# Kernel tuning notes

Hardware: AMD Instinct MI355X
Metric: run time of the kernel (lower is better)

Reference implementation:

```python
import jax, jax.numpy as jnp
import numpy as np

SEG = 4      # segment_size
H = 8        # n_heads
D = 1024     # d_model
B = 8
S = 4096


def setup_inputs() -> dict:
    key = jax.random.key(0)
    ks = jax.random.split(key, 9)
    s = 0.02  # init scale for weights
    return {
        "x": jax.random.normal(ks[0], (B, S, D), dtype=jnp.float32),
        "proj_qk_w": jax.random.normal(ks[1], (D, D), dtype=jnp.float32) * s,
        "proj_qk_b": jax.random.normal(ks[2], (D,), dtype=jnp.float32) * s,
        "proj_v_w": jax.random.normal(ks[3], (D, D), dtype=jnp.float32) * s,
        "proj_v_b": jax.random.normal(ks[4], (D,), dtype=jnp.float32) * s,
        "in_proj_w": jax.random.normal(ks[5], (3 * D, D), dtype=jnp.float32) * s,
        "in_proj_b": jax.random.normal(ks[6], (3 * D,), dtype=jnp.float32) * s,
        "out_proj_w": jax.random.normal(ks[7], (D, D), dtype=jnp.float32) * s,
        "out_proj_b": jax.random.normal(ks[8], (D,), dtype=jnp.float32) * s,
    }


def reference(x, proj_qk_w, proj_qk_b, proj_v_w, proj_v_b,
              in_proj_w, in_proj_b, out_proj_w, out_proj_b):
    b, seq_len, d = x.shape
    hd = d // H
    # torch: pad = seg - S % seg  (pads a full segment when S % seg == 0)
    pad = SEG - seq_len % SEG
    x = jnp.concatenate([x, x[:, :pad]], axis=1)          # [b, T, d]
    T = seq_len + pad
    a = T // SEG
    # cat(chunk(x, a, dim=1), dim=0): block-major stacking -> [a*b, SEG, d]
    xb = x.reshape(b, a, SEG, d).transpose(1, 0, 2, 3).reshape(a * b, SEG, d)

    # extra projections (same qk projection used for query and key)
    qk_in = xb @ proj_qk_w.T + proj_qk_b                   # [a*b, SEG, d]
    v_in = xb @ proj_v_w.T + proj_v_b

    # nn.MultiheadAttention in-projection
    wq, wk, wv = jnp.split(in_proj_w, 3, axis=0)
    bq, bk, bv = jnp.split(in_proj_b, 3)
    q = (qk_in @ wq.T + bq).reshape(a * b, SEG, H, hd)
    k = (qk_in @ wk.T + bk).reshape(a * b, SEG, H, hd)
    v = (v_in @ wv.T + bv).reshape(a * b, SEG, H, hd)

    scale = 1.0 / np.sqrt(hd).astype(np.float32)
    scores = jnp.einsum('nqhd,nkhd->nhqk', q * scale, k)   # [a*b, H, SEG, SEG]
    # diagonal exclusion mask (True on the diagonal = masked)
    diag = jnp.eye(SEG, dtype=bool)
    scores = jnp.where(diag[None, None], jnp.finfo(scores.dtype).min, scores)
    attn = jax.nn.softmax(scores, axis=-1)
    o = jnp.einsum('nhqk,nkhd->nqhd', attn, v).reshape(a * b, SEG, d)
    o = o @ out_proj_w.T + out_proj_b                      # [a*b, SEG, d]

    # cat(chunk(x, a, dim=0), dim=1): invert the block stacking
    out = o.reshape(a, b, SEG, d).transpose(1, 0, 2, 3).reshape(b, T, d)
    return out[:, :seq_len]
```

## Files before the change

### kernel.cpp

```cpp
#include <hip/hip_runtime.h>
#include <hip/hip_bf16.h>

typedef __bf16 bf16x8 __attribute__((ext_vector_type(8)));
typedef float f32x4 __attribute__((ext_vector_type(4)));

__device__ __forceinline__ float bf2f(unsigned int u) {
    unsigned int x = u << 16;
    return __builtin_bit_cast(float, x);
}
__device__ __forceinline__ unsigned short f2bf(float f) {
    unsigned int x = __builtin_bit_cast(unsigned int, f);
    x += 0x7fffu + ((x >> 16) & 1u);
    return (unsigned short)(x >> 16);
}

__device__ __forceinline__ void gld_lds16(const unsigned short* g, unsigned short* s) {
    __builtin_amdgcn_global_load_lds((const __attribute__((address_space(1))) void*)g,
                                     (__attribute__((address_space(3))) void*)s, 16, 0, 0);
}

template<bool OUT_F32>
__global__ __launch_bounds__(512) void gemm256(
    const unsigned short* __restrict__ A, int lda,
    const unsigned short* __restrict__ B,
    const float* __restrict__ bias,
    void* __restrict__ C, int N, int K, int nx)
{
    extern __shared__ char smem[];
    const int tid   = threadIdx.x;
    const int lane  = tid & 63;
    const int wave  = tid >> 6;
    const int wm    = (wave >> 2) * 128;
    const int wn    = (wave & 3) * 64;
    const int lrow  = lane & 15;
    const int lquad = lane >> 4;

    int L = (int)blockIdx.x;
    L = (L & 7) * ((int)gridDim.x >> 3) + (L >> 3);
    const long bm = (long)(L / nx) * 256;
    const long bn = (long)(L % nx) * 256;

    const int srow = (lane & 7) + ((lane >> 5) << 3);
    const int scol = ((lane >> 3) & 3) * 8;
    const unsigned short* Asrc0 = A + (bm + wave * 16 + srow) * (long)lda + scol;
    const unsigned short* Asrc1 = A + (bm + (8 + wave) * 16 + srow) * (long)lda + scol;
    const unsigned short* Bsrc0 = B + (bn + wave * 16 + srow) * (long)K + scol;
    const unsigned short* Bsrc1 = B + (bn + (8 + wave) * 16 + srow) * (long)K + scol;

    const int dA0 = wave * 1024 + lane * 16;
    const int dA1 = (8 + wave) * 1024 + lane * 16;
    const int dB0 = 16384 + dA0;
    const int dB1 = 16384 + dA1;

    const int rdoff = (lrow & 7) * 16 + (lrow >> 3) * 512 + lquad * 128;

    f32x4 acc[8][4];
#pragma unroll
    for (int i = 0; i < 8; i++)
#pragma unroll
        for (int j = 0; j < 4; j++)
            acc[i][j] = (f32x4){0.f, 0.f, 0.f, 0.f};

    const int NU = K >> 5;

    auto stageA = [&](int su, int slot) {
        char* sb = smem + (size_t)(slot * 32768);
        gld_lds16(Asrc0 + su * 32, (unsigned short*)(sb + dA0));
        gld_lds16(Asrc1 + su * 32, (unsigned short*)(sb + dA1));
    };
    auto stageB = [&](int su, int slot) {
        char* sb = smem + (size_t)(slot * 32768);
        gld_lds16(Bsrc0 + su * 32, (unsigned short*)(sb + dB0));
        gld_lds16(Bsrc1 + su * 32, (unsigned short*)(sb + dB1));
    };

    stageA(0, 0); stageB(0, 0);
    stageA(1, 1); stageB(1, 1);
    stageA(2, 2); stageB(2, 2);
    asm volatile("s_waitcnt vmcnt(8)\n\ts_barrier" ::: "memory");

    for (int u = 0; u < NU; ++u) {
        char* sl = smem + (size_t)((u & 3) * 32768);
        const int us   = (u + 3 < NU) ? (u + 3) : (NU - 1);
        const int slot = (u + 3) & 3;
        bf16x8 af0[4], af1[4], bq[4];

#pragma unroll
        for (int j = 0; j < 4; j++)
            bq[j] = *(const bf16x8*)(sl + 16384 + ((wn >> 4) + j) * 1024 + rdoff);
#pragma unroll
        for (int i = 0; i < 4; i++)
            af0[i] = *(const bf16x8*)(sl + ((wm >> 4) + i) * 1024 + rdoff);
        stageA(us, slot);
        __builtin_amdgcn_sched_barrier(0);
        __builtin_amdgcn_s_barrier();
        asm volatile("s_waitcnt lgkmcnt(0)" ::: "memory");
        __builtin_amdgcn_sched_barrier(0);
        __builtin_amdgcn_s_setprio(1);
#pragma unroll
        for (int i = 0; i < 4; i++)
#pragma unroll
            for (int j = 0; j < 4; j++)
                acc[i][j] = __builtin_amdgcn_mfma_f32_16x16x32_bf16(bq[j], af0[i], acc[i][j], 0, 0, 0);
        __builtin_amdgcn_s_setprio(0);
        __builtin_amdgcn_sched_barrier(0);
        __builtin_amdgcn_s_barrier();

#pragma unroll
        for (int i = 0; i < 4; i++)
            af1[i] = *(const bf16x8*)(sl + ((wm >> 4) + 4 + i) * 1024 + rdoff);
        stageB(us, slot);
        __builtin_amdgcn_sched_barrier(0);
        __builtin_amdgcn_s_barrier();
        asm volatile("s_waitcnt lgkmcnt(0)" ::: "memory");
        __builtin_amdgcn_sched_barrier(0);
        __builtin_amdgcn_s_setprio(1);
#pragma unroll
        for (int i = 0; i < 4; i++)
#pragma unroll
            for (int j = 0; j < 4; j++)
                acc[4 + i][j] = __builtin_amdgcn_mfma_f32_16x16x32_bf16(bq[j], af1[i], acc[4 + i][j], 0, 0, 0);
        __builtin_amdgcn_s_setprio(0);
        __builtin_amdgcn_sched_barrier(0);
        asm volatile("s_waitcnt vmcnt(8)\n\ts_barrier" ::: "memory");
    }

    asm volatile("s_waitcnt vmcnt(0)" ::: "memory");

#pragma unroll
    for (int i = 0; i < 8; i++) {
        const long row = bm + wm + i * 16 + lrow;
#pragma unroll
        for (int j = 0; j < 4; j++) {
            const int colb = (int)bn + wn + j * 16 + lquad * 4;
            float4 b4 = bias ? ((const float4*)bias)[colb >> 2]
                             : make_float4(0.f, 0.f, 0.f, 0.f);
            const float v0 = acc[i][j][0] + b4.x;
            const float v1 = acc[i][j][1] + b4.y;
            const float v2 = acc[i][j][2] + b4.z;
            const float v3 = acc[i][j][3] + b4.w;
            if (OUT_F32) {
                *(float4*)&((float*)C)[row * (long)N + colb] = make_float4(v0, v1, v2, v3);
            } else {
                unsigned int lo = (unsigned int)f2bf(v0) | ((unsigned int)f2bf(v1) << 16);
                unsigned int hi = (unsigned int)f2bf(v2) | ((unsigned int)f2bf(v3) << 16);
                *(uint2*)&((unsigned short*)C)[row * (long)N + colb] = make_uint2(lo, hi);
            }
        }
    }
}

template<bool OUT_F32>
__global__ __launch_bounds__(256) void gemm_bt(
    const unsigned short* __restrict__ A, int lda,
    const unsigned short* __restrict__ B,
    const unsigned short* __restrict__ B2, long bsplit,
    const float* __restrict__ bias,
    void* __restrict__ C, int N, int K)
{
    __shared__ unsigned short As[128 * 32];
    __shared__ unsigned short Bs[128 * 32];
    const int tid   = threadIdx.x;
    const int lane  = tid & 63;
    const int wave  = tid >> 6;
    const int wm    = (wave >> 1) * 64;
    const int wn    = (wave & 1) * 64;
    const int lrow  = lane & 15;
    const int lquad = lane >> 4;
    const long bm = (long)blockIdx.y * 128;
    const long bn = (long)blockIdx.x * 128;
    const unsigned short* Bp = (bm >= bsplit) ? B2 : B;

    f32x4 acc[4][4];
#pragma unroll
    for (int i = 0; i < 4; i++)
#pragma unroll
        for (int j = 0; j < 4; j++)
            acc[i][j] = (f32x4){0.f, 0.f, 0.f, 0.f};

    const int r0 = tid >> 2;
    const int c0 = (tid & 3) * 8;
    const unsigned short* Ag0 = A + (bm + r0) * (long)lda + c0;
    const unsigned short* Ag1 = A + (bm + r0 + 64) * (long)lda + c0;
    const unsigned short* Bg0 = Bp + (bn + r0) * (long)K + c0;
    const unsigned short* Bg1 = Bp + (bn + r0 + 64) * (long)K + c0;
    unsigned short* As0 = &As[tid * 8];
    unsigned short* As1 = &As[tid * 8 + 2048];
    unsigned short* Bs0 = &Bs[tid * 8];
    unsigned short* Bs1 = &Bs[tid * 8 + 2048];

    for (int k0 = 0; k0 < K; k0 += 32) {
        gld_lds16(Ag0 + k0, As0);
        gld_lds16(Ag1 + k0, As1);
        gld_lds16(Bg0 + k0, Bs0);
        gld_lds16(Bg1 + k0, Bs1);
        __syncthreads();
        bf16x8 af[4], bq[4];
#pragma unroll
        for (int i = 0; i < 4; i++)
            af[i] = *(const bf16x8*)&As[(wm + i * 16 + lrow) * 32 + lquad * 8];
#pragma unroll
        for (int j = 0; j < 4; j++)
            bq[j] = *(const bf16x8*)&Bs[(wn + j * 16 + lrow) * 32 + lquad * 8];
#pragma unroll
        for (int i = 0; i < 4; i++)
#pragma unroll
            for (int j = 0; j < 4; j++)
                acc[i][j] = __builtin_amdgcn_mfma_f32_16x16x32_bf16(bq[j], af[i], acc[i][j], 0, 0, 0);
        __syncthreads();
    }

#pragma unroll
    for (int i = 0; i < 4; i++) {
        const long row = bm + wm + i * 16 + lrow;
#pragma unroll
        for (int j = 0; j < 4; j++) {
            const int colb = (int)bn + wn + j * 16 + lquad * 4;
            float4 b4 = bias ? ((const float4*)bias)[colb >> 2]
                             : make_float4(0.f, 0.f, 0.f, 0.f);
            const float v0 = acc[i][j][0] + b4.x;
            const float v1 = acc[i][j][1] + b4.y;
            const float v2 = acc[i][j][2] + b4.z;
            const float v3 = acc[i][j][3] + b4.w;
            if (OUT_F32) {
                *(float4*)&((float*)C)[row * (long)N + colb] = make_float4(v0, v1, v2, v3);
            } else {
                unsigned int lo = (unsigned int)f2bf(v0) | ((unsigned int)f2bf(v1) << 16);
                unsigned int hi = (unsigned int)f2bf(v2) | ((unsigned int)f2bf(v3) << 16);
                *(uint2*)&((unsigned short*)C)[row * (long)N + colb] = make_uint2(lo, hi);
            }
        }
    }
}

__global__ __launch_bounds__(256) void attn4(
    const unsigned short* __restrict__ QKV,
    unsigned short* __restrict__ O)
{
    const int wave = threadIdx.x >> 6;
    const int lane = threadIdx.x & 63;
    const int half = lane >> 5;
    const int l    = lane & 31;
    const int gh = blockIdx.x * 8 + wave * 2 + half;
    const int g = gh >> 3, h = gh & 7;
    const long row0 = (long)g * 4;
    const int d0 = h * 128 + l * 4;
    const float scale = 0.08838834764831845f;

    float q[4][4], k[4][4], v[4][4];
#pragma unroll
    for (int i = 0; i < 4; i++) {
        const unsigned short* base = QKV + (row0 + i) * 3072 + d0;
        uint2 uq = *(const uint2*)base;
        uint2 uk = *(const uint2*)(base + 1024);
        uint2 uv = *(const uint2*)(base + 2048);
        q[i][0] = bf2f(uq.x & 0xffffu); q[i][1] = bf2f(uq.x >> 16);
        q[i][2] = bf2f(uq.y & 0xffffu); q[i][3] = bf2f(uq.y >> 16);
        k[i][0] = bf2f(uk.x & 0xffffu); k[i][1] = bf2f(uk.x >> 16);
        k[i][2] = bf2f(uk.y & 0xffffu); k[i][3] = bf2f(uk.y >> 16);
        v[i][0] = bf2f(uv.x & 0xffffu); v[i][1] = bf2f(uv.x >> 16);
        v[i][2] = bf2f(uv.y & 0xffffu); v[i][3] = bf2f(uv.y >> 16);
    }
    float s[4][4];
#pragma unroll
    for (int i = 0; i < 4; i++)
#pragma unroll
        for (int j = 0; j < 4; j++)
            s[i][j] = q[i][0] * k[j][0] + q[i][1] * k[j][1]
                    + q[i][2] * k[j][2] + q[i][3] * k[j][3];
#pragma unroll
    for (int m = 1; m < 32; m <<= 1)
#pragma unroll
        for (int i = 0; i < 4; i++)
#pragma unroll
            for (int j = 0; j < 4; j++)
                s[i][j] += __shfl_xor(s[i][j], m, 64);

#pragma unroll
    for (int i = 0; i < 4; i++) {
        float mx = -3.0e38f;
#pragma unroll
        for (int j = 0; j < 4; j++)
            if (j != i) mx = fmaxf(mx, s[i][j] * scale);
        float p[4], den = 0.f;
#pragma unroll
        for (int j = 0; j < 4; j++) {
            p[j] = (j == i) ? 0.f : __expf(s[i][j] * scale - mx);
            den += p[j];
        }
        const float inv = 1.f / den;
        float o0 = 0.f, o1 = 0.f, o2 = 0.f, o3 = 0.f;
#pragma unroll
        for (int j = 0; j < 4; j++) {
            const float a = p[j] * inv;
            o0 += a * v[j][0]; o1 += a * v[j][1];
            o2 += a * v[j][2]; o3 += a * v[j][3];
        }
        unsigned int lo = (unsigned int)f2bf(o0) | ((unsigned int)f2bf(o1) << 16);
        unsigned int hi = (unsigned int)f2bf(o2) | ((unsigned int)f2bf(o3) << 16);
        *(uint2*)(O + (row0 + i) * 1024 + d0) = make_uint2(lo, hi);
    }
}

__global__ __launch_bounds__(256) void cvt_bf16(const float* __restrict__ in,
                                                unsigned short* __restrict__ out, int n4)
{
    int i = blockIdx.x * blockDim.x + threadIdx.x;
    if (i >= n4) return;
    float4 v = ((const float4*)in)[i];
    unsigned int a = (unsigned int)f2bf(v.x) | ((unsigned int)f2bf(v.y) << 16);
    unsigned int b = (unsigned int)f2bf(v.z) | ((unsigned int)f2bf(v.w) << 16);
    ((uint2*)out)[i] = make_uint2(a, b);
}

__global__ __launch_bounds__(256) void prep_w(
    const float* __restrict__ win,  unsigned short* __restrict__ win16,
    const float* __restrict__ wout, unsigned short* __restrict__ wo16,
    const float* __restrict__ wqk,  unsigned short* __restrict__ wqkT,
    const float* __restrict__ wv,   unsigned short* __restrict__ wvT,
    const float* __restrict__ bqk,  const float* __restrict__ bv,
    const float* __restrict__ bin,  float* __restrict__ bbig)
{
    __shared__ unsigned short tile[64][65];
    const int bid = blockIdx.x;
    if (bid < 4096) {
        int i = bid * 256 + threadIdx.x;
        const float* in;
        unsigned short* out;
        int j;
        if (i < 786432) { in = win; out = win16; j = i; }
        else            { in = wout; out = wo16; j = i - 786432; }
        float4 v = ((const float4*)in)[j];
        unsigned int a = (unsigned int)f2bf(v.x) | ((unsigned int)f2bf(v.y) << 16);
        unsigned int b = (unsigned int)f2bf(v.z) | ((unsigned int)f2bf(v.w) << 16);
        ((uint2*)out)[j] = make_uint2(a, b);
    } else if (bid < 4608) {
        const int b2 = bid - 4096;
        const int z = b2 >> 8, rem = b2 & 255;
        const int bx = (rem & 15) * 64, by = (rem >> 4) * 64;
        const float* in = z ? wv : wqk;
        unsigned short* out = z ? wvT : wqkT;
        const int tx = threadIdx.x & 63, ty = threadIdx.x >> 6;
        for (int r = ty; r < 64; r += 4)
            tile[r][tx] = f2bf(in[(long)(by + r) * 1024 + bx + tx]);
        __syncthreads();
        for (int r = ty; r < 64; r += 4)
            out[(long)(bx + r) * 1024 + by + tx] = tile[tx][r];
    } else {
        const int row = (bid - 4608) * 4 + (threadIdx.x >> 6);
        const int lane = threadIdx.x & 63;
        const float* b = (row < 2048) ? bqk : bv;
        float s = 0.f;
        for (int t = lane; t < 1024; t += 64) s += win[(long)row * 1024 + t] * b[t];
#pragma unroll
        for (int m = 1; m < 64; m <<= 1) s += __shfl_xor(s, m, 64);
        if (lane == 0) bbig[row] = s + bin[row];
    }
}

extern "C" void kernel_launch(void* const* d_in, const int* in_sizes, int n_in,
                              void* d_out, int out_size, void* d_ws, size_t ws_size,
                              hipStream_t stream)
{
    (void)in_sizes; (void)n_in; (void)out_size; (void)ws_size;
    const float* x    = (const float*)d_in[0];
    const float* wqk  = (const float*)d_in[1];
    const float* bqk  = (const float*)d_in[2];
    const float* wv   = (const float*)d_in[3];
    const float* bv   = (const float*)d_in[4];
    const float* win  = (const float*)d_in[5];
    const float* bin  = (const float*)d_in[6];
    const float* wout = (const float*)d_in[7];
    const float* bout = (const float*)d_in[8];

    char* ws = (char*)d_ws;
    unsigned short* buf0  = (unsigned short*)ws;
    unsigned short* qkv   = (unsigned short*)(ws + (64ll << 20));
    unsigned short* win16 = (unsigned short*)(ws + (256ll << 20));
    unsigned short* wqkT  = (unsigned short*)(ws + (262ll << 20));
    unsigned short* wvT   = (unsigned short*)(ws + (264ll << 20));
    unsigned short* wbig  = (unsigned short*)(ws + (266ll << 20));
    unsigned short* wo16  = (unsigned short*)(ws + (272ll << 20));
    float*          bbig  = (float*)(ws + (274ll << 20));
    unsigned short* o16   = buf0;

    hipFuncSetAttribute(reinterpret_cast<const void*>(&gemm256<false>),
                        hipFuncAttributeMaxDynamicSharedMemorySize, 131072);
    hipFuncSetAttribute(reinterpret_cast<const void*>(&gemm256<true>),
                        hipFuncAttributeMaxDynamicSharedMemorySize, 131072);

    dim3 blk(256);
    cvt_bf16<<<32768, 256, 0, stream>>>(x, buf0, 8388608);
    prep_w<<<5376, blk, 0, stream>>>(win, win16, wout, wo16,
                                     wqk, wqkT, wv, wvT, bqk, bv, bin, bbig);

    gemm_bt<false><<<dim3(8, 24), blk, 0, stream>>>(win16, 1024, wqkT, wvT, 2048,
                                                    nullptr, wbig, 1024, 1024);

    gemm256<false><<<dim3(1536), 512, 131072, stream>>>(buf0, 1024, wbig,
                                                        bbig, qkv, 3072, 1024, 12);

    attn4<<<8192, blk, 0, stream>>>(qkv, o16);

    gemm256<true><<<dim3(512), 512, 131072, stream>>>(o16, 1024, wo16,
                                                      bout, d_out, 1024, 1024, 4);
}
```

Measured before the change: 686.2 us.

## Pipeline weight-fold GEMM with triple-buffered LDS and merge input conversion kernels

Reworks the small 3072x1024 weight-folding GEMM into a triple-buffered LDS pipeline that prefetches two K-steps ahead with vmcnt waits. It also uses a swizzled LDS layout, raised MFMA priority and a block index remap. It also folds the x fp32-to-bf16 conversion into the weight-prep kernel to drop a launch. This targets load latency stalls and launch overhead, but the weight GEMM is a small share of total time next to the large projection GEMMs.

```diff
diff --git a/kernel.cpp b/kernel.cpp
--- a/kernel.cpp
+++ b/kernel.cpp
@@ -150,16 +150,14 @@
     }
 }
 
-template<bool OUT_F32>
-__global__ __launch_bounds__(256) void gemm_bt(
+__global__ __launch_bounds__(256, 3) void gemm128f(
     const unsigned short* __restrict__ A, int lda,
     const unsigned short* __restrict__ B,
     const unsigned short* __restrict__ B2, long bsplit,
-    const float* __restrict__ bias,
-    void* __restrict__ C, int N, int K)
+    unsigned short* __restrict__ C, int N, int K, int nbn)
 {
-    __shared__ unsigned short As[128 * 32];
-    __shared__ unsigned short Bs[128 * 32];
+    __shared__ uint4 smem4[3072];
+    char* smem = (char*)smem4;
     const int tid   = threadIdx.x;
     const int lane  = tid & 63;
     const int wave  = tid >> 6;
@@ -167,10 +165,27 @@
     const int wn    = (wave & 1) * 64;
     const int lrow  = lane & 15;
     const int lquad = lane >> 4;
-    const long bm = (long)blockIdx.y * 128;
-    const long bn = (long)blockIdx.x * 128;
+
+    int L = (int)blockIdx.x;
+    L = (L & 7) * ((int)gridDim.x >> 3) + (L >> 3);
+    const long bm = (long)(L / nbn) * 128;
+    const long bn = (long)(L % nbn) * 128;
     const unsigned short* Bp = (bm >= bsplit) ? B2 : B;
 
+    const int srow = (lane & 7) + ((lane >> 5) << 3);
+    const int scol = ((lane >> 3) & 3) * 8;
+    const unsigned short* Ag0 = A + (bm + wave * 16 + srow) * (long)lda + scol;
+    const unsigned short* Ag1 = A + (bm + (wave + 4) * 16 + srow) * (long)lda + scol;
+    const unsigned short* Bg0 = Bp + (bn + wave * 16 + srow) * (long)K + scol;
+    const unsigned short* Bg1 = Bp + (bn + (wave + 4) * 16 + srow) * (long)K + scol;
+
+    const int dA0 = wave * 1024 + lane * 16;
+    const int dA1 = dA0 + 4096;
+    const int dB0 = 8192 + dA0;
+    const int dB1 = 8192 + dA1;
+
+    const int rdoff = (lrow & 7) * 16 + (lrow >> 3) * 512 + lquad * 128;
+
     f32x4 acc[4][4];
 #pragma unroll
     for (int i = 0; i < 4; i++)
@@ -178,37 +193,48 @@
         for (int j = 0; j < 4; j++)
             acc[i][j] = (f32x4){0.f, 0.f, 0.f, 0.f};
 
-    const int r0 = tid >> 2;
-    const int c0 = (tid & 3) * 8;
-    const unsigned short* Ag0 = A + (bm + r0) * (long)lda + c0;
-    const unsigned short* Ag1 = A + (bm + r0 + 64) * (long)lda + c0;
-    const unsigned short* Bg0 = Bp + (bn + r0) * (long)K + c0;
-    const unsigned short* Bg1 = Bp + (bn + r0 + 64) * (long)K + c0;
-    unsigned short* As0 = &As[tid * 8];
-    unsigned short* As1 = &As[tid * 8 + 2048];
-    unsigned short* Bs0 = &Bs[tid * 8];
-    unsigned short* Bs1 = &Bs[tid * 8 + 2048];
-
-    for (int k0 = 0; k0 < K; k0 += 32) {
-        gld_lds16(Ag0 + k0, As0);
-        gld_lds16(Ag1 + k0, As1);
-        gld_lds16(Bg0 + k0, Bs0);
-        gld_lds16(Bg1 + k0, Bs1);
-        __syncthreads();
+    const int NU = K >> 5;
+
+    auto stage = [&](int su, char* sb) {
+        gld_lds16(Ag0 + su * 32, (unsigned short*)(sb + dA0));
+        gld_lds16(Ag1 + su * 32, (unsigned short*)(sb + dA1));
+        gld_lds16(Bg0 + su * 32, (unsigned short*)(sb + dB0));
+        gld_lds16(Bg1 + su * 32, (unsigned short*)(sb + dB1));
+    };
+
+    stage(0, smem);
+    stage(1, smem + 16384);
+    asm volatile("s_waitcnt vmcnt(4)\n\ts_barrier" ::: "memory");
+
+    int cs = 0, ws = 2;
+    for (int u = 0; u < NU; ++u) {
+        const char* sl = smem + cs * 16384;
+        char* sw = smem + ws * 16384;
+        const int us = (u + 2 < NU) ? (u + 2) : (NU - 1);
         bf16x8 af[4], bq[4];
-#pragma unroll
-        for (int i = 0; i < 4; i++)
-            af[i] = *(const bf16x8*)&As[(wm + i * 16 + lrow) * 32 + lquad * 8];
-#pragma unroll
-        for (int j = 0; j < 4; j++)
-            bq[j] = *(const bf16x8*)&Bs[(wn + j * 16 + lrow) * 32 + lquad * 8];
+
+#pragma unroll
+        for (int j = 0; j < 4; j++)
+            bq[j] = *(const bf16x8*)(sl + 8192 + ((wn >> 4) + j) * 1024 + rdoff);
+#pragma unroll
+        for (int i = 0; i < 4; i++)
+            af[i] = *(const bf16x8*)(sl + ((wm >> 4) + i) * 1024 + rdoff);
+        stage(us, sw);
+
+        __builtin_amdgcn_s_setprio(1);
 #pragma unroll
         for (int i = 0; i < 4; i++)
 #pragma unroll
             for (int j = 0; j < 4; j++)
                 acc[i][j] = __builtin_amdgcn_mfma_f32_16x16x32_bf16(bq[j], af[i], acc[i][j], 0, 0, 0);
-        __syncthreads();
-    }
+        __builtin_amdgcn_s_setprio(0);
+
+        asm volatile("s_waitcnt vmcnt(4)\n\ts_barrier" ::: "memory");
+        cs = (cs == 2) ? 0 : cs + 1;
+        ws = (ws == 2) ? 0 : ws + 1;
+    }
+
+    asm volatile("s_waitcnt vmcnt(0)" ::: "memory");
 
 #pragma unroll
     for (int i = 0; i < 4; i++) {
@@ -216,19 +242,9 @@
 #pragma unroll
         for (int j = 0; j < 4; j++) {
             const int colb = (int)bn + wn + j * 16 + lquad * 4;
-            float4 b4 = bias ? ((const float4*)bias)[colb >> 2]
-                             : make_float4(0.f, 0.f, 0.f, 0.f);
-            const float v0 = acc[i][j][0] + b4.x;
-            const float v1 = acc[i][j][1] + b4.y;
-            const float v2 = acc[i][j][2] + b4.z;
-            const float v3 = acc[i][j][3] + b4.w;
-            if (OUT_F32) {
-                *(float4*)&((float*)C)[row * (long)N + colb] = make_float4(v0, v1, v2, v3);
-            } else {
-                unsigned int lo = (unsigned int)f2bf(v0) | ((unsigned int)f2bf(v1) << 16);
-                unsigned int hi = (unsigned int)f2bf(v2) | ((unsigned int)f2bf(v3) << 16);
-                *(uint2*)&((unsigned short*)C)[row * (long)N + colb] = make_uint2(lo, hi);
-            }
+            unsigned int lo = (unsigned int)f2bf(acc[i][j][0]) | ((unsigned int)f2bf(acc[i][j][1]) << 16);
+            unsigned int hi = (unsigned int)f2bf(acc[i][j][2]) | ((unsigned int)f2bf(acc[i][j][3]) << 16);
+            *(uint2*)&C[row * (long)N + colb] = make_uint2(lo, hi);
         }
     }
 }
@@ -302,18 +318,8 @@
     }
 }
 
-__global__ __launch_bounds__(256) void cvt_bf16(const float* __restrict__ in,
-                                                unsigned short* __restrict__ out, int n4)
-{
-    int i = blockIdx.x * blockDim.x + threadIdx.x;
-    if (i >= n4) return;
-    float4 v = ((const float4*)in)[i];
-    unsigned int a = (unsigned int)f2bf(v.x) | ((unsigned int)f2bf(v.y) << 16);
-    unsigned int b = (unsigned int)f2bf(v.z) | ((unsigned int)f2bf(v.w) << 16);
-    ((uint2*)out)[i] = make_uint2(a, b);
-}
-
-__global__ __launch_bounds__(256) void prep_w(
+__global__ __launch_bounds__(256) void prep_all(
+    const float* __restrict__ x,    unsigned short* __restrict__ x16,
     const float* __restrict__ win,  unsigned short* __restrict__ win16,
     const float* __restrict__ wout, unsigned short* __restrict__ wo16,
     const float* __restrict__ wqk,  unsigned short* __restrict__ wqkT,
@@ -323,8 +329,14 @@
 {
     __shared__ unsigned short tile[64][65];
     const int bid = blockIdx.x;
-    if (bid < 4096) {
+    if (bid < 32768) {
         int i = bid * 256 + threadIdx.x;
+        float4 v = ((const float4*)x)[i];
+        unsigned int a = (unsigned int)f2bf(v.x) | ((unsigned int)f2bf(v.y) << 16);
+        unsigned int b = (unsigned int)f2bf(v.z) | ((unsigned int)f2bf(v.w) << 16);
+        ((uint2*)x16)[i] = make_uint2(a, b);
+    } else if (bid < 36864) {
+        int i = (bid - 32768) * 256 + threadIdx.x;
         const float* in;
         unsigned short* out;
         int j;
@@ -334,8 +346,8 @@
         unsigned int a = (unsigned int)f2bf(v.x) | ((unsigned int)f2bf(v.y) << 16);
         unsigned int b = (unsigned int)f2bf(v.z) | ((unsigned int)f2bf(v.w) << 16);
         ((uint2*)out)[j] = make_uint2(a, b);
-    } else if (bid < 4608) {
-        const int b2 = bid - 4096;
+    } else if (bid < 37376) {
+        const int b2 = bid - 36864;
         const int z = b2 >> 8, rem = b2 & 255;
         const int bx = (rem & 15) * 64, by = (rem >> 4) * 64;
         const float* in = z ? wv : wqk;
@@ -347,7 +359,7 @@
         for (int r = ty; r < 64; r += 4)
             out[(long)(bx + r) * 1024 + by + tx] = tile[tx][r];
     } else {
-        const int row = (bid - 4608) * 4 + (threadIdx.x >> 6);
+        const int row = (bid - 37376) * 4 + (threadIdx.x >> 6);
         const int lane = threadIdx.x & 63;
         const float* b = (row < 2048) ? bqk : bv;
         float s = 0.f;
@@ -390,12 +402,11 @@
                         hipFuncAttributeMaxDynamicSharedMemorySize, 131072);
 
     dim3 blk(256);
-    cvt_bf16<<<32768, 256, 0, stream>>>(x, buf0, 8388608);
-    prep_w<<<5376, blk, 0, stream>>>(win, win16, wout, wo16,
-                                     wqk, wqkT, wv, wvT, bqk, bv, bin, bbig);
-
-    gemm_bt<false><<<dim3(8, 24), blk, 0, stream>>>(win16, 1024, wqkT, wvT, 2048,
-                                                    nullptr, wbig, 1024, 1024);
+    prep_all<<<38144, blk, 0, stream>>>(x, buf0, win, win16, wout, wo16,
+                                        wqk, wqkT, wv, wvT, bqk, bv, bin, bbig);
+
+    gemm128f<<<dim3(192), blk, 0, stream>>>(win16, 1024, wqkT, wvT, 2048,
+                                            wbig, 1024, 1024, 8);
 
     gemm256<false><<<dim3(1536), 512, 131072, stream>>>(buf0, 1024, wbig,
                                                         bbig, qkv, 3072, 1024, 12);
```

New measurement: 674.6 us. No clear change (-1.7%).
